# Performance work log

Hardware: AMD Instinct MI355X
Metric: run time of the kernel (lower is better)

The kernel has to match this reference:

```python
import jax, jax.numpy as jnp
import numpy as np

LORA_SCALING = 1.0 / 4.0  # lora_alpha / lora_rank
NUM_HEADS = 16
HEAD_DIM = 64
ROPE_BASE = 20000.0


def rotate_half(x):
    x1, x2 = jnp.split(x, 2, axis=-1)
    return jnp.concatenate([-x2, x1], axis=-1)


def setup_inputs() -> dict:
    key = jax.random.key(0)
    ks = jax.random.split(key, 8)
    B, S, D = 8, 1024, 1024
    hidden_states = jax.random.normal(ks[0], (B, S, D), jnp.float32)
    attention_mask = jnp.zeros((B, 1, 1, S), jnp.float32)
    # real rotary tables (HF style: duplicated half-dim freqs)
    inv_freq = 1.0 / (ROPE_BASE ** (jnp.arange(0, HEAD_DIM, 2, dtype=jnp.float32) / HEAD_DIM))
    t = jnp.arange(S, dtype=jnp.float32)
    freqs = jnp.outer(t, inv_freq)                      # [S, hd/2]
    emb = jnp.concatenate([freqs, freqs], axis=-1)      # [S, hd]
    cos = jnp.broadcast_to(jnp.cos(emb)[None], (B, S, HEAD_DIM))
    sin = jnp.broadcast_to(jnp.sin(emb)[None], (B, S, HEAD_DIM))
    adapter_mask = jax.random.randint(ks[1], (B,), 0, 5, jnp.int32)
    Wqkv_weight = jax.random.normal(ks[2], (3 * D, D), jnp.float32) * 0.02
    Wqkv_bias = jax.random.normal(ks[3], (3 * D,), jnp.float32) * 0.02
    lora_A = jax.random.normal(ks[4], (5, 4, D), jnp.float32) * 0.02
    lora_B = jax.random.normal(ks[5], (5, 3 * D, 4), jnp.float32) * 0.02
    return dict(hidden_states=hidden_states, attention_mask=attention_mask,
                cos=cos, sin=sin, adapter_mask=adapter_mask,
                Wqkv_weight=Wqkv_weight, Wqkv_bias=Wqkv_bias,
                lora_A=lora_A, lora_B=lora_B)


def reference(hidden_states, attention_mask, cos, sin, adapter_mask,
              Wqkv_weight, Wqkv_bias, lora_A, lora_B):
    B, S, D = hidden_states.shape
    H, hd = NUM_HEADS, HEAD_DIM
    # fused QKV projection with per-task LoRA (gather adapters per batch row)
    base = jnp.einsum('bsd,od->bso', hidden_states, Wqkv_weight) + Wqkv_bias
    A_t = lora_A[adapter_mask]                    # [B, r, D]
    B_t = lora_B[adapter_mask]                    # [B, 3D, r]
    lo = jnp.einsum('bsd,brd->bsr', hidden_states, A_t)
    delta = jnp.einsum('bsr,bor->bso', lo, B_t) * LORA_SCALING
    qkv = (base + delta).reshape(B, S, 3, H, hd)
    q = qkv[:, :, 0].transpose(0, 2, 1, 3)        # [B,H,S,hd]
    k = qkv[:, :, 1].transpose(0, 2, 1, 3)
    v = qkv[:, :, 2].transpose(0, 2, 1, 3)
    # inline RoPE
    c = cos[:, None, :, :]
    s = sin[:, None, :, :]
    q = q * c + rotate_half(q) * s
    k = k * c + rotate_half(k) * s
    # eager SDPA
    scaling = hd ** -0.5
    scores = jnp.einsum('bhqd,bhkd->bhqk', q, k) * scaling + attention_mask
    attn = jax.nn.softmax(scores, axis=-1)
    out = jnp.einsum('bhqk,bhkd->bhqd', attn, v)
    return out.transpose(0, 2, 1, 3).reshape(B, S, H * hd)
```

## Files before the change

### kernel.cpp

```cpp
#include <hip/hip_runtime.h>
#include <hip/hip_bf16.h>
#include <stdint.h>

typedef __attribute__((ext_vector_type(8))) short short8;
typedef __attribute__((ext_vector_type(4))) float f32x4;
typedef unsigned short ushort_t;

#define MFMA16(a, b, c) __builtin_amdgcn_mfma_f32_16x16x32_bf16((a), (b), (c), 0, 0, 0)
#define EXP2F(x) __builtin_amdgcn_exp2f(x)
#define BAR() __builtin_amdgcn_s_barrier()


__device__ __forceinline__ float bf2f(unsigned short u) {
    union { unsigned int i; float f; } x; x.i = ((unsigned int)u) << 16; return x.f;
}
__device__ __forceinline__ unsigned short f2bf(float f) {
    union { float f; unsigned int i; } x; x.f = f;
    unsigned int i = x.i;
    i = i + 0x7FFFu + ((i >> 16) & 1u);
    return (unsigned short)(i >> 16);
}
__device__ __forceinline__ unsigned int pack2(float a, float b) {
    return (unsigned int)f2bf(a) | ((unsigned int)f2bf(b) << 16);
}
__device__ __forceinline__ void glds16(const void* gsrc, void* ldst) {
    __builtin_amdgcn_global_load_lds(
        (const __attribute__((address_space(1))) unsigned int*)gsrc,
        (__attribute__((address_space(3))) unsigned int*)ldst, 16, 0, 0);
}

__global__ __launch_bounds__(64) void prep_kernel(
    const float* __restrict__ hidden,
    const float* __restrict__ W,
    const float* __restrict__ loraA,
    const int* __restrict__ adapter_mask,
    ushort_t* __restrict__ Hb,
    ushort_t* __restrict__ Wb,
    float4* __restrict__ lo)
{
    int blk = blockIdx.x;
    int lane = threadIdx.x;
    if (blk < 8192) {
        int b = blk >> 10;
        int a = adapter_mask[b];
        const float* hp = hidden + (size_t)blk * 1024 + lane * 16;
        float hv[16];
        for (int j = 0; j < 16; ++j) hv[j] = hp[j];
        uint4 p0, p1;
        p0.x = pack2(hv[0], hv[1]);  p0.y = pack2(hv[2], hv[3]);
        p0.z = pack2(hv[4], hv[5]);  p0.w = pack2(hv[6], hv[7]);
        p1.x = pack2(hv[8], hv[9]);  p1.y = pack2(hv[10], hv[11]);
        p1.z = pack2(hv[12], hv[13]); p1.w = pack2(hv[14], hv[15]);
        uint4* hd = (uint4*)(Hb + (size_t)blk * 1024 + lane * 16);
        hd[0] = p0; hd[1] = p1;
        const float* Ap = loraA + (size_t)a * 4096 + lane * 16;
        float acc[4];
        for (int r = 0; r < 4; ++r) {
            const float* ap = Ap + r * 1024;
            float s = 0.f;
            for (int j = 0; j < 16; ++j) s += hv[j] * ap[j];
            acc[r] = s;
        }
        for (int off = 32; off > 0; off >>= 1)
            for (int r = 0; r < 4; ++r) acc[r] += __shfl_xor(acc[r], off);
        if (lane == 0) lo[blk] = make_float4(acc[0], acc[1], acc[2], acc[3]);
    } else {
        int row = blk - 8192;
        const float* wp = W + (size_t)row * 1024 + lane * 16;
        float wv[16];
        for (int j = 0; j < 16; ++j) wv[j] = wp[j];
        uint4 p0, p1;
        p0.x = pack2(wv[0], wv[1]);  p0.y = pack2(wv[2], wv[3]);
        p0.z = pack2(wv[4], wv[5]);  p0.w = pack2(wv[6], wv[7]);
        p1.x = pack2(wv[8], wv[9]);  p1.y = pack2(wv[10], wv[11]);
        p1.z = pack2(wv[12], wv[13]); p1.w = pack2(wv[14], wv[15]);
        uint4* wd = (uint4*)(Wb + (size_t)row * 1024 + lane * 16);
        wd[0] = p0; wd[1] = p1;
    }
}

__global__ __launch_bounds__(512, 2) void qkv_gemm_kernel(
    const ushort_t* __restrict__ Hb,
    const ushort_t* __restrict__ Wb,
    const float* __restrict__ bias,
    const float4* __restrict__ lo,
    const float* __restrict__ loraB,
    const int* __restrict__ adapter_mask,
    const float* __restrict__ cosp,
    const float* __restrict__ sinp,
    ushort_t* __restrict__ qw,
    ushort_t* __restrict__ kw,
    ushort_t* __restrict__ vt)
{
    __shared__ __align__(16) ushort_t As[2][16384];
    __shared__ __align__(16) ushort_t Bs[2][16384];
    int tid = threadIdx.x;
    int wave = tid >> 6, lane = tid & 63, quad = lane >> 4, l16 = lane & 15;
    int wm = wave >> 2, wn = wave & 3;

    int wg = (blockIdx.x & 7) * 48 + (blockIdx.x >> 3);
    int bx = wg % 12, by = wg / 12;
    int n0 = bx * 256;
    int m0 = by * 256;

    int r_ = tid >> 3, c_ = (tid & 7) ^ (r_ & 7);
    const ushort_t* pA0 = Hb + (size_t)(m0 +   0 + r_) * 1024 + c_ * 8;
    const ushort_t* pA1 = Hb + (size_t)(m0 +  64 + r_) * 1024 + c_ * 8;
    const ushort_t* pA2 = Hb + (size_t)(m0 + 128 + r_) * 1024 + c_ * 8;
    const ushort_t* pA3 = Hb + (size_t)(m0 + 192 + r_) * 1024 + c_ * 8;
    const ushort_t* pB0 = Wb + (size_t)(n0 +   0 + r_) * 1024 + c_ * 8;
    const ushort_t* pB1 = Wb + (size_t)(n0 +  64 + r_) * 1024 + c_ * 8;
    const ushort_t* pB2 = Wb + (size_t)(n0 + 128 + r_) * 1024 + c_ * 8;
    const ushort_t* pB3 = Wb + (size_t)(n0 + 192 + r_) * 1024 + c_ * 8;
    char* stA0 = (char*)&As[0][0] + wave * 1024;
    char* stB0 = (char*)&Bs[0][0] + wave * 1024;

    f32x4 acc[8][4];
#pragma unroll
    for (int i = 0; i < 8; ++i)
#pragma unroll
        for (int j = 0; j < 4; ++j) acc[i][j] = (f32x4)0.f;

    glds16(pB0, stB0);          glds16(pB1, stB0 + 8192);
    glds16(pB2, stB0 + 16384);  glds16(pB3, stB0 + 24576);
    glds16(pA0, stA0);          glds16(pA1, stA0 + 8192);
    glds16(pA2, stA0 + 16384);  glds16(pA3, stA0 + 24576);
    glds16(pB0 + 64, stB0 + 32768);          glds16(pB1 + 64, stB0 + 32768 + 8192);
    glds16(pB2 + 64, stB0 + 32768 + 16384);  glds16(pB3 + 64, stB0 + 32768 + 24576);

#pragma unroll 2
    for (int t = 0; t < 16; ++t) {
        int cur = t & 1;
        const char* rdA = (const char*)&As[0][0] + cur * 32768;
        const char* rdB = (const char*)&Bs[0][0] + cur * 32768;
        char* sA = stA0 + (cur ^ 1) * 32768;
        char* sB = stB0 + cur * 32768;
        int kA = (t + 1) << 6;
        int kB = (t + 2) << 6;

        if (t < 15) { asm volatile("s_waitcnt vmcnt(4)" ::: "memory"); }
        else        { asm volatile("s_waitcnt vmcnt(0)" ::: "memory"); }
        BAR();
        if (t < 15) {
            glds16(pA0 + kA, sA);          glds16(pA1 + kA, sA + 8192);
            glds16(pA2 + kA, sA + 16384);  glds16(pA3 + kA, sA + 24576);
        }
        short8 bfr[4][2];
#pragma unroll
        for (int ni = 0; ni < 4; ++ni) {
            int rb = ni * 16 + l16;
            bfr[ni][0] = *(const short8*)(rdB + wn * 8192 + (rb * 8 + ((quad    ) ^ (rb & 7))) * 16);
            bfr[ni][1] = *(const short8*)(rdB + wn * 8192 + (rb * 8 + ((quad + 4) ^ (rb & 7))) * 16);
        }
        asm volatile("s_waitcnt lgkmcnt(0)" ::: "memory");
        BAR();
        if (t < 14) {
            glds16(pB0 + kB, sB);          glds16(pB1 + kB, sB + 8192);
            glds16(pB2 + kB, sB + 16384);  glds16(pB3 + kB, sB + 24576);
        }
        __builtin_amdgcn_s_setprio(1);
#pragma unroll
        for (int mi = 0; mi < 8; ++mi) {
            int u = wm * 2 + (mi >> 2);
            int rr = (mi & 3) * 16 + l16;
            short8 a0 = *(const short8*)(rdA + u * 8192 + (rr * 8 + ((quad    ) ^ (rr & 7))) * 16);
            short8 a1 = *(const short8*)(rdA + u * 8192 + (rr * 8 + ((quad + 4) ^ (rr & 7))) * 16);
            acc[mi][0] = MFMA16(a0, bfr[0][0], acc[mi][0]);
            acc[mi][1] = MFMA16(a0, bfr[1][0], acc[mi][1]);
            acc[mi][2] = MFMA16(a0, bfr[2][0], acc[mi][2]);
            acc[mi][3] = MFMA16(a0, bfr[3][0], acc[mi][3]);
            acc[mi][0] = MFMA16(a1, bfr[0][1], acc[mi][0]);
            acc[mi][1] = MFMA16(a1, bfr[1][1], acc[mi][1]);
            acc[mi][2] = MFMA16(a1, bfr[2][1], acc[mi][2]);
            acc[mi][3] = MFMA16(a1, bfr[3][1], acc[mi][3]);
        }
        __builtin_amdgcn_s_setprio(0);
    }

    int t_qkv = n0 >> 10;
    int b = m0 >> 10;
    int a_idx = adapter_mask[b];
    float bi[4], bb[4][4];
    int cpos[4], chh[4];
#pragma unroll
    for (int ni = 0; ni < 4; ++ni) {
        int c = n0 + wn * 64 + ni * 16 + l16;
        bi[ni] = bias[c];
        const float* Bp = loraB + ((size_t)a_idx * 3072 + c) * 4;
        bb[ni][0] = Bp[0]; bb[ni][1] = Bp[1]; bb[ni][2] = Bp[2]; bb[ni][3] = Bp[3];
        cpos[ni] = c & 63; chh[ni] = (c >> 6) & 15;
    }
#pragma unroll
    for (int mi = 0; mi < 8; ++mi) {
        float vals[4][4];
        int mrow0 = m0 + wm * 128 + mi * 16 + quad * 4;
#pragma unroll
        for (int r = 0; r < 4; ++r) {
            float4 lov = lo[mrow0 + r];
#pragma unroll
            for (int ni = 0; ni < 4; ++ni)
                vals[r][ni] = acc[mi][ni][r] + bi[ni]
                      + 0.25f * (lov.x * bb[ni][0] + lov.y * bb[ni][1]
                               + lov.z * bb[ni][2] + lov.w * bb[ni][3]);
        }
        int s0 = mrow0 & 1023;
        if (t_qkv < 2) {
#pragma unroll
            for (int r = 0; r < 4; ++r) {
                int s = s0 + r;
                size_t cb = ((size_t)b * 1024 + s) * 64;
                float cA = cosp[cb + l16],      sA_ = sinp[cb + l16];
                float cB = cosp[cb + 16 + l16], sB_ = sinp[cb + 16 + l16];
                float w0 = vals[r][0] * cA - vals[r][2] * sA_;
                float w2 = vals[r][2] * cA + vals[r][0] * sA_;
                float w1 = vals[r][1] * cB - vals[r][3] * sB_;
                float w3 = vals[r][3] * cB + vals[r][1] * sB_;
                float v[4] = {w0, w1, w2, w3};
#pragma unroll
                for (int ni = 0; ni < 4; ++ni) {
                    size_t bh = (size_t)b * 16 + chh[ni];
                    ushort_t ob = f2bf(v[ni]);
                    if (t_qkv == 0) qw[(bh * 1024 + s) * 64 + cpos[ni]] = ob;
                    else            kw[(bh * 1024 + s) * 64 + cpos[ni]] = ob;
                }
            }
        } else {
#pragma unroll
            for (int ni = 0; ni < 4; ++ni) {
                uint2 pk;
                pk.x = pack2(vals[0][ni], vals[1][ni]);
                pk.y = pack2(vals[2][ni], vals[3][ni]);
                size_t bh = (size_t)b * 16 + chh[ni];
                *(uint2*)&vt[(bh * 64 + cpos[ni]) * 1024 + s0] = pk;
            }
        }
    }
}

__global__ __launch_bounds__(256) void attn_kernel(
    const ushort_t* __restrict__ qw,
    const ushort_t* __restrict__ kw,
    const ushort_t* __restrict__ vt,
    const float* __restrict__ mask,
    float* __restrict__ out)
{
    __shared__ __align__(16) ushort_t Kt[3][4096];
    __shared__ __align__(16) ushort_t Vt[3][4096];
    __shared__ __align__(16) ushort_t Ps[4][32][72];
    __shared__ float mlds[1024];
    const float KSCALE = 0.125f * 1.44269504f;
    int tid = threadIdx.x;
    int wave = tid >> 6, lane = tid & 63, quad = lane >> 4, l16 = lane & 15;
    int id = blockIdx.x;
    int qt = id >> 7;
    int bh = id & 127;
    int b = bh >> 4, h = bh & 15;
    size_t base = (size_t)bh * 65536;
    int q0 = qt * 128 + wave * 32;

    for (int i = tid; i < 1024; i += 256) mlds[i] = mask[b * 1024 + i] * 1.44269504f;

    const ushort_t* kbase = kw + base;
    const ushort_t* vbase = vt + base;

    int n0 = tid, n1 = tid + 256;
    int r0 = n0 >> 3, c0 = (n0 & 7) ^ (r0 & 7);
    int r1 = n1 >> 3, c1 = (n1 & 7) ^ (r1 & 7);

    short8 qf[2][2];
    for (int mt = 0; mt < 2; ++mt)
        for (int kt = 0; kt < 2; ++kt)
            qf[mt][kt] = *(const short8*)(qw + base + (size_t)(q0 + mt * 16 + l16) * 64 + kt * 32 + quad * 8);

    f32x4 oacc[2][4], sum_acc[2];
    for (int mt = 0; mt < 2; ++mt) {
        sum_acc[mt] = (f32x4)0.f;
        for (int nt = 0; nt < 4; ++nt) oacc[mt][nt] = (f32x4)0.f;
    }

    short8 ones;
    for (int j = 0; j < 8; ++j) ones[j] = (short)0x3F80;

    __syncthreads();

    int koff[4][2], voff[4][2];
    for (int nt = 0; nt < 4; ++nt)
        for (int kt = 0; kt < 2; ++kt) {
            int rr = nt * 16 + l16;
            int cc = (kt * 4 + quad) ^ (rr & 7);
            koff[nt][kt] = (rr * 8 + cc) * 8;
            voff[nt][kt] = (rr * 8 + cc) * 8;
        }

    {
        char* kd = (char*)&Kt[0][0] + wave * 1024;
        char* vd = (char*)&Vt[0][0] + wave * 1024;
        glds16(kbase + (size_t)r0 * 64 + c0 * 8, kd);
        glds16(kbase + (size_t)r1 * 64 + c1 * 8, kd + 4096);
        glds16(vbase + (size_t)r0 * 1024 + c0 * 8, vd);
        glds16(vbase + (size_t)r1 * 1024 + c1 * 8, vd + 4096);
        kd = (char*)&Kt[1][0] + wave * 1024;
        vd = (char*)&Vt[1][0] + wave * 1024;
        glds16(kbase + (size_t)(64 + r0) * 64 + c0 * 8, kd);
        glds16(kbase + (size_t)(64 + r1) * 64 + c1 * 8, kd + 4096);
        glds16(vbase + (size_t)r0 * 1024 + 64 + c0 * 8, vd);
        glds16(vbase + (size_t)r1 * 1024 + 64 + c1 * 8, vd + 4096);
    }

    const ushort_t* kR  = &Kt[0][0];  const ushort_t* vR  = &Vt[0][0];
    const ushort_t* kN1 = &Kt[1][0];  const ushort_t* vN1 = &Vt[1][0];
    const ushort_t* kN2 = &Kt[2][0];  const ushort_t* vN2 = &Vt[2][0];

    for (int it = 0; it < 16; ++it) {
        int kt0 = it * 64;
        if (it < 15) { asm volatile("s_waitcnt vmcnt(4)" ::: "memory"); }
        else         { asm volatile("s_waitcnt vmcnt(0)" ::: "memory"); }
        BAR();
        __builtin_amdgcn_sched_barrier(0);
        if (it < 14) {
            int kn = kt0 + 128;
            char* kd = (char*)kN2 + wave * 1024;
            char* vd = (char*)vN2 + wave * 1024;
            glds16(kbase + (size_t)(kn + r0) * 64 + c0 * 8, kd);
            glds16(kbase + (size_t)(kn + r1) * 64 + c1 * 8, kd + 4096);
            glds16(vbase + (size_t)r0 * 1024 + kn + c0 * 8, vd);
            glds16(vbase + (size_t)r1 * 1024 + kn + c1 * 8, vd + 4096);
        }
        short8 kf[4][2];
        for (int nt = 0; nt < 4; ++nt)
            for (int kt = 0; kt < 2; ++kt)
                kf[nt][kt] = *(const short8*)&kR[koff[nt][kt]];
        f32x4 sacc[2][4];
        for (int mt = 0; mt < 2; ++mt)
            for (int nt = 0; nt < 4; ++nt) {
                f32x4 z = (f32x4)0.f;
                z = MFMA16(qf[mt][0], kf[nt][0], z);
                z = MFMA16(qf[mt][1], kf[nt][1], z);
                sacc[mt][nt] = z;
            }
        float mv[4];
        for (int nt = 0; nt < 4; ++nt) mv[nt] = mlds[kt0 + nt * 16 + l16];
        for (int mt = 0; mt < 2; ++mt)
            for (int nt = 0; nt < 4; ++nt)
                for (int r = 0; r < 4; ++r) {
                    float p = EXP2F(sacc[mt][nt][r] * KSCALE + mv[nt]);
                    Ps[wave][mt * 16 + quad * 4 + r][nt * 16 + l16] = f2bf(p);
                }
        short8 pf[2][2];
        for (int mt = 0; mt < 2; ++mt)
            for (int kt = 0; kt < 2; ++kt)
                pf[mt][kt] = *(const short8*)&Ps[wave][mt * 16 + l16][kt * 32 + quad * 8];
        short8 vf[4][2];
        for (int nt = 0; nt < 4; ++nt)
            for (int kt = 0; kt < 2; ++kt)
                vf[nt][kt] = *(const short8*)&vR[voff[nt][kt]];
        for (int mt = 0; mt < 2; ++mt) {
            for (int nt = 0; nt < 4; ++nt) {
                oacc[mt][nt] = MFMA16(pf[mt][0], vf[nt][0], oacc[mt][nt]);
                oacc[mt][nt] = MFMA16(pf[mt][1], vf[nt][1], oacc[mt][nt]);
            }
            sum_acc[mt] = MFMA16(pf[mt][0], ones, sum_acc[mt]);
            sum_acc[mt] = MFMA16(pf[mt][1], ones, sum_acc[mt]);
        }
        const ushort_t* tk = kR; kR = kN1; kN1 = kN2; kN2 = tk;
        const ushort_t* tv = vR; vR = vN1; vN1 = vN2; vN2 = tv;
    }

    for (int mt = 0; mt < 2; ++mt) {
        for (int r = 0; r < 4; ++r) {
            float inv = 1.f / sum_acc[mt][r];
            int s = q0 + mt * 16 + quad * 4 + r;
            size_t ob = ((size_t)b * 1024 + s) * 1024 + h * 64;
            for (int nt = 0; nt < 4; ++nt)
                out[ob + nt * 16 + l16] = oacc[mt][nt][r] * inv;
        }
    }
}

extern "C" void kernel_launch(void* const* d_in, const int* in_sizes, int n_in,
                              void* d_out, int out_size, void* d_ws, size_t ws_size,
                              hipStream_t stream)
{
    const float* hidden = (const float*)d_in[0];
    const float* mask   = (const float*)d_in[1];
    const float* cosp   = (const float*)d_in[2];
    const float* sinp   = (const float*)d_in[3];
    const int* adapter_mask = (const int*)d_in[4];
    const float* W      = (const float*)d_in[5];
    const float* bias   = (const float*)d_in[6];
    const float* loraA  = (const float*)d_in[7];
    const float* loraB  = (const float*)d_in[8];
    float* out = (float*)d_out;

    char* ws = (char*)d_ws;
    float4* lo = (float4*)ws;
    ushort_t* qw = (ushort_t*)(ws + (1 << 20));
    ushort_t* kw = qw + (size_t)8 * 16 * 1024 * 64;
    ushort_t* vt = kw + (size_t)8 * 16 * 1024 * 64;

    ushort_t* Hb = (ushort_t*)d_out;
    ushort_t* Wb = Hb + (size_t)8192 * 1024;

    prep_kernel<<<11264, 64, 0, stream>>>(hidden, W, loraA, adapter_mask, Hb, Wb, lo);
    qkv_gemm_kernel<<<384, 512, 0, stream>>>(Hb, Wb, bias, lo, loraB, adapter_mask,
                                             cosp, sinp, qw, kw, vt);
    attn_kernel<<<1024, 256, 0, stream>>>(qw, kw, vt, mask, out);
}
```

Measured before the change: 251.0 us.

## Shrink QKV GEMM tiles to 256x128 with BK=32 and 4-wave blocks

Reworks the QKV projection GEMM from 256x256 tiles with 8 waves and a K-step of 64 into 256x128 tiles with 4 waves and a K-step of 32, launching 768 blocks instead of 384. LDS use per block drops, the XOR swizzle changes to match the 64-byte rows, and up to three blocks may now share a CU. The aim is better occupancy and less tail imbalance. In exchange, each B tile is reused less, the loop runs twice as many iterations with barriers, and the MFMA priority hints are removed.

```diff
diff --git a/kernel.cpp b/kernel.cpp
--- a/kernel.cpp
+++ b/kernel.cpp
@@ -79,7 +79,7 @@
     }
 }
 
-__global__ __launch_bounds__(512, 2) void qkv_gemm_kernel(
+__global__ __launch_bounds__(256, 3) void qkv_gemm_kernel(
     const ushort_t* __restrict__ Hb,
     const ushort_t* __restrict__ Wb,
     const float* __restrict__ bias,
@@ -92,28 +92,31 @@
     ushort_t* __restrict__ kw,
     ushort_t* __restrict__ vt)
 {
-    __shared__ __align__(16) ushort_t As[2][16384];
-    __shared__ __align__(16) ushort_t Bs[2][16384];
+    __shared__ __align__(16) ushort_t As[2][8192];
+    __shared__ __align__(16) ushort_t Bs[2][4096];
     int tid = threadIdx.x;
     int wave = tid >> 6, lane = tid & 63, quad = lane >> 4, l16 = lane & 15;
-    int wm = wave >> 2, wn = wave & 3;
-
-    int wg = (blockIdx.x & 7) * 48 + (blockIdx.x >> 3);
-    int bx = wg % 12, by = wg / 12;
-    int n0 = bx * 256;
+    int wm = wave >> 1, wn = wave & 1;
+
+    int wg = (blockIdx.x & 7) * 96 + (blockIdx.x >> 3);
+    int bx = wg % 24, by = wg / 24;
+    int n0 = bx * 128;
     int m0 = by * 256;
 
-    int r_ = tid >> 3, c_ = (tid & 7) ^ (r_ & 7);
-    const ushort_t* pA0 = Hb + (size_t)(m0 +   0 + r_) * 1024 + c_ * 8;
-    const ushort_t* pA1 = Hb + (size_t)(m0 +  64 + r_) * 1024 + c_ * 8;
-    const ushort_t* pA2 = Hb + (size_t)(m0 + 128 + r_) * 1024 + c_ * 8;
-    const ushort_t* pA3 = Hb + (size_t)(m0 + 192 + r_) * 1024 + c_ * 8;
-    const ushort_t* pB0 = Wb + (size_t)(n0 +   0 + r_) * 1024 + c_ * 8;
-    const ushort_t* pB1 = Wb + (size_t)(n0 +  64 + r_) * 1024 + c_ * 8;
-    const ushort_t* pB2 = Wb + (size_t)(n0 + 128 + r_) * 1024 + c_ * 8;
-    const ushort_t* pB3 = Wb + (size_t)(n0 + 192 + r_) * 1024 + c_ * 8;
-    char* stA0 = (char*)&As[0][0] + wave * 1024;
-    char* stB0 = (char*)&Bs[0][0] + wave * 1024;
+    int rr = tid >> 2;
+    int cg = (tid & 3) ^ ((tid >> 3) & 3);
+    const ushort_t* pA0 = Hb + (size_t)(m0 +   0 + rr) * 1024 + cg * 8;
+    const ushort_t* pA1 = Hb + (size_t)(m0 +  64 + rr) * 1024 + cg * 8;
+    const ushort_t* pA2 = Hb + (size_t)(m0 + 128 + rr) * 1024 + cg * 8;
+    const ushort_t* pA3 = Hb + (size_t)(m0 + 192 + rr) * 1024 + cg * 8;
+    const ushort_t* pB0 = Wb + (size_t)(n0 +   0 + rr) * 1024 + cg * 8;
+    const ushort_t* pB1 = Wb + (size_t)(n0 +  64 + rr) * 1024 + cg * 8;
+    char* stA = (char*)&As[0][0] + wave * 1024;
+    char* stB = (char*)&Bs[0][0] + wave * 1024;
+
+    int slotoff = (quad ^ ((l16 >> 1) & 3)) * 16;
+    int bA = (wm * 128 + l16) * 64 + slotoff;
+    int bB = (wn * 64 + l16) * 64 + slotoff;
 
     f32x4 acc[8][4];
 #pragma unroll
@@ -121,60 +124,45 @@
 #pragma unroll
         for (int j = 0; j < 4; ++j) acc[i][j] = (f32x4)0.f;
 
-    glds16(pB0, stB0);          glds16(pB1, stB0 + 8192);
-    glds16(pB2, stB0 + 16384);  glds16(pB3, stB0 + 24576);
-    glds16(pA0, stA0);          glds16(pA1, stA0 + 8192);
-    glds16(pA2, stA0 + 16384);  glds16(pA3, stA0 + 24576);
-    glds16(pB0 + 64, stB0 + 32768);          glds16(pB1 + 64, stB0 + 32768 + 8192);
-    glds16(pB2 + 64, stB0 + 32768 + 16384);  glds16(pB3 + 64, stB0 + 32768 + 24576);
+    glds16(pB0, stB);          glds16(pB1, stB + 4096);
+    glds16(pA0, stA);          glds16(pA1, stA + 4096);
+    glds16(pA2, stA + 8192);   glds16(pA3, stA + 12288);
+    glds16(pB0 + 32, stB + 8192);  glds16(pB1 + 32, stB + 8192 + 4096);
 
 #pragma unroll 2
-    for (int t = 0; t < 16; ++t) {
+    for (int t = 0; t < 32; ++t) {
         int cur = t & 1;
-        const char* rdA = (const char*)&As[0][0] + cur * 32768;
-        const char* rdB = (const char*)&Bs[0][0] + cur * 32768;
-        char* sA = stA0 + (cur ^ 1) * 32768;
-        char* sB = stB0 + cur * 32768;
-        int kA = (t + 1) << 6;
-        int kB = (t + 2) << 6;
-
-        if (t < 15) { asm volatile("s_waitcnt vmcnt(4)" ::: "memory"); }
+        const char* rdA = (const char*)&As[0][0] + cur * 16384;
+        const char* rdB = (const char*)&Bs[0][0] + cur * 8192;
+        char* sA = stA + (cur ^ 1) * 16384;
+        char* sB = stB + cur * 8192;
+        int kA = (t + 1) * 32;
+        int kB = (t + 2) * 32;
+
+        if (t < 31) { asm volatile("s_waitcnt vmcnt(2)" ::: "memory"); }
         else        { asm volatile("s_waitcnt vmcnt(0)" ::: "memory"); }
         BAR();
-        if (t < 15) {
-            glds16(pA0 + kA, sA);          glds16(pA1 + kA, sA + 8192);
-            glds16(pA2 + kA, sA + 16384);  glds16(pA3 + kA, sA + 24576);
-        }
-        short8 bfr[4][2];
-#pragma unroll
-        for (int ni = 0; ni < 4; ++ni) {
-            int rb = ni * 16 + l16;
-            bfr[ni][0] = *(const short8*)(rdB + wn * 8192 + (rb * 8 + ((quad    ) ^ (rb & 7))) * 16);
-            bfr[ni][1] = *(const short8*)(rdB + wn * 8192 + (rb * 8 + ((quad + 4) ^ (rb & 7))) * 16);
-        }
+        if (t < 31) {
+            glds16(pA0 + kA, sA);          glds16(pA1 + kA, sA + 4096);
+            glds16(pA2 + kA, sA + 8192);   glds16(pA3 + kA, sA + 12288);
+        }
+        short8 bfr[4];
+#pragma unroll
+        for (int ni = 0; ni < 4; ++ni)
+            bfr[ni] = *(const short8*)(rdB + bB + ni * 1024);
         asm volatile("s_waitcnt lgkmcnt(0)" ::: "memory");
         BAR();
-        if (t < 14) {
-            glds16(pB0 + kB, sB);          glds16(pB1 + kB, sB + 8192);
-            glds16(pB2 + kB, sB + 16384);  glds16(pB3 + kB, sB + 24576);
-        }
-        __builtin_amdgcn_s_setprio(1);
+        if (t < 30) {
+            glds16(pB0 + kB, sB);          glds16(pB1 + kB, sB + 4096);
+        }
 #pragma unroll
         for (int mi = 0; mi < 8; ++mi) {
-            int u = wm * 2 + (mi >> 2);
-            int rr = (mi & 3) * 16 + l16;
-            short8 a0 = *(const short8*)(rdA + u * 8192 + (rr * 8 + ((quad    ) ^ (rr & 7))) * 16);
-            short8 a1 = *(const short8*)(rdA + u * 8192 + (rr * 8 + ((quad + 4) ^ (rr & 7))) * 16);
-            acc[mi][0] = MFMA16(a0, bfr[0][0], acc[mi][0]);
-            acc[mi][1] = MFMA16(a0, bfr[1][0], acc[mi][1]);
-            acc[mi][2] = MFMA16(a0, bfr[2][0], acc[mi][2]);
-            acc[mi][3] = MFMA16(a0, bfr[3][0], acc[mi][3]);
-            acc[mi][0] = MFMA16(a1, bfr[0][1], acc[mi][0]);
-            acc[mi][1] = MFMA16(a1, bfr[1][1], acc[mi][1]);
-            acc[mi][2] = MFMA16(a1, bfr[2][1], acc[mi][2]);
-            acc[mi][3] = MFMA16(a1, bfr[3][1], acc[mi][3]);
-        }
-        __builtin_amdgcn_s_setprio(0);
+            short8 a = *(const short8*)(rdA + bA + mi * 1024);
+            acc[mi][0] = MFMA16(a, bfr[0], acc[mi][0]);
+            acc[mi][1] = MFMA16(a, bfr[1], acc[mi][1]);
+            acc[mi][2] = MFMA16(a, bfr[2], acc[mi][2]);
+            acc[mi][3] = MFMA16(a, bfr[3], acc[mi][3]);
+        }
     }
 
     int t_qkv = n0 >> 10;
@@ -402,7 +390,7 @@
     ushort_t* Wb = Hb + (size_t)8192 * 1024;
 
     prep_kernel<<<11264, 64, 0, stream>>>(hidden, W, loraA, adapter_mask, Hb, Wb, lo);
-    qkv_gemm_kernel<<<384, 512, 0, stream>>>(Hb, Wb, bias, lo, loraB, adapter_mask,
+    qkv_gemm_kernel<<<768, 256, 0, stream>>>(Hb, Wb, bias, lo, loraB, adapter_mask,
                                              cosp, sinp, qw, kw, vt);
     attn_kernel<<<1024, 256, 0, stream>>>(qw, kw, vt, mask, out);
 }
```

Result: slower. 270.3 us (+7.7%).

## Load K/V fragments directly from global in attention and pack prep blocks

Applied to the files above, without the earlier changes.

The attention kernel drops its triple-buffered LDS staging of K and V tiles, including the async global-to-LDS loads, waitcnt and barriers. Each wave now reads its MFMA K and V fragments straight from global memory, relying on L1/L2 to serve the reuse across the four waves in a block. This removes barrier synchronisation and LDS traffic, but loses explicit prefetch overlap and may add redundant global reads. Separately, the prep kernel packs four 64-thread rows into one 256-thread block to cut the block count.

```diff
diff --git a/kernel.cpp b/kernel.cpp
--- a/kernel.cpp
+++ b/kernel.cpp
@@ -29,7 +29,7 @@
         (__attribute__((address_space(3))) unsigned int*)ldst, 16, 0, 0);
 }
 
-__global__ __launch_bounds__(64) void prep_kernel(
+__global__ __launch_bounds__(256) void prep_kernel(
     const float* __restrict__ hidden,
     const float* __restrict__ W,
     const float* __restrict__ loraA,
@@ -38,8 +38,9 @@
     ushort_t* __restrict__ Wb,
     float4* __restrict__ lo)
 {
-    int blk = blockIdx.x;
-    int lane = threadIdx.x;
+    int tid = threadIdx.x;
+    int blk = blockIdx.x * 4 + (tid >> 6);
+    int lane = tid & 63;
     if (blk < 8192) {
         int b = blk >> 10;
         int a = adapter_mask[b];
@@ -244,8 +245,6 @@
     const float* __restrict__ mask,
     float* __restrict__ out)
 {
-    __shared__ __align__(16) ushort_t Kt[3][4096];
-    __shared__ __align__(16) ushort_t Vt[3][4096];
     __shared__ __align__(16) ushort_t Ps[4][32][72];
     __shared__ float mlds[1024];
     const float KSCALE = 0.125f * 1.44269504f;
@@ -263,10 +262,6 @@
     const ushort_t* kbase = kw + base;
     const ushort_t* vbase = vt + base;
 
-    int n0 = tid, n1 = tid + 256;
-    int r0 = n0 >> 3, c0 = (n0 & 7) ^ (r0 & 7);
-    int r1 = n1 >> 3, c1 = (n1 & 7) ^ (r1 & 7);
-
     short8 qf[2][2];
     for (int mt = 0; mt < 2; ++mt)
         for (int kt = 0; kt < 2; ++kt)
@@ -283,53 +278,13 @@
 
     __syncthreads();
 
-    int koff[4][2], voff[4][2];
-    for (int nt = 0; nt < 4; ++nt)
-        for (int kt = 0; kt < 2; ++kt) {
-            int rr = nt * 16 + l16;
-            int cc = (kt * 4 + quad) ^ (rr & 7);
-            koff[nt][kt] = (rr * 8 + cc) * 8;
-            voff[nt][kt] = (rr * 8 + cc) * 8;
-        }
-
-    {
-        char* kd = (char*)&Kt[0][0] + wave * 1024;
-        char* vd = (char*)&Vt[0][0] + wave * 1024;
-        glds16(kbase + (size_t)r0 * 64 + c0 * 8, kd);
-        glds16(kbase + (size_t)r1 * 64 + c1 * 8, kd + 4096);
-        glds16(vbase + (size_t)r0 * 1024 + c0 * 8, vd);
-        glds16(vbase + (size_t)r1 * 1024 + c1 * 8, vd + 4096);
-        kd = (char*)&Kt[1][0] + wave * 1024;
-        vd = (char*)&Vt[1][0] + wave * 1024;
-        glds16(kbase + (size_t)(64 + r0) * 64 + c0 * 8, kd);
-        glds16(kbase + (size_t)(64 + r1) * 64 + c1 * 8, kd + 4096);
-        glds16(vbase + (size_t)r0 * 1024 + 64 + c0 * 8, vd);
-        glds16(vbase + (size_t)r1 * 1024 + 64 + c1 * 8, vd + 4096);
-    }
-
-    const ushort_t* kR  = &Kt[0][0];  const ushort_t* vR  = &Vt[0][0];
-    const ushort_t* kN1 = &Kt[1][0];  const ushort_t* vN1 = &Vt[1][0];
-    const ushort_t* kN2 = &Kt[2][0];  const ushort_t* vN2 = &Vt[2][0];
-
     for (int it = 0; it < 16; ++it) {
         int kt0 = it * 64;
-        if (it < 15) { asm volatile("s_waitcnt vmcnt(4)" ::: "memory"); }
-        else         { asm volatile("s_waitcnt vmcnt(0)" ::: "memory"); }
-        BAR();
-        __builtin_amdgcn_sched_barrier(0);
-        if (it < 14) {
-            int kn = kt0 + 128;
-            char* kd = (char*)kN2 + wave * 1024;
-            char* vd = (char*)vN2 + wave * 1024;
-            glds16(kbase + (size_t)(kn + r0) * 64 + c0 * 8, kd);
-            glds16(kbase + (size_t)(kn + r1) * 64 + c1 * 8, kd + 4096);
-            glds16(vbase + (size_t)r0 * 1024 + kn + c0 * 8, vd);
-            glds16(vbase + (size_t)r1 * 1024 + kn + c1 * 8, vd + 4096);
-        }
         short8 kf[4][2];
         for (int nt = 0; nt < 4; ++nt)
             for (int kt = 0; kt < 2; ++kt)
-                kf[nt][kt] = *(const short8*)&kR[koff[nt][kt]];
+                kf[nt][kt] = *(const short8*)(kbase
+                    + (size_t)(kt0 + nt * 16 + l16) * 64 + kt * 32 + quad * 8);
         f32x4 sacc[2][4];
         for (int mt = 0; mt < 2; ++mt)
             for (int nt = 0; nt < 4; ++nt) {
@@ -353,7 +308,8 @@
         short8 vf[4][2];
         for (int nt = 0; nt < 4; ++nt)
             for (int kt = 0; kt < 2; ++kt)
-                vf[nt][kt] = *(const short8*)&vR[voff[nt][kt]];
+                vf[nt][kt] = *(const short8*)(vbase
+                    + (size_t)(nt * 16 + l16) * 1024 + kt0 + kt * 32 + quad * 8);
         for (int mt = 0; mt < 2; ++mt) {
             for (int nt = 0; nt < 4; ++nt) {
                 oacc[mt][nt] = MFMA16(pf[mt][0], vf[nt][0], oacc[mt][nt]);
@@ -362,8 +318,6 @@
             sum_acc[mt] = MFMA16(pf[mt][0], ones, sum_acc[mt]);
             sum_acc[mt] = MFMA16(pf[mt][1], ones, sum_acc[mt]);
         }
-        const ushort_t* tk = kR; kR = kN1; kN1 = kN2; kN2 = tk;
-        const ushort_t* tv = vR; vR = vN1; vN1 = vN2; vN2 = tv;
     }
 
     for (int mt = 0; mt < 2; ++mt) {
@@ -401,7 +355,7 @@
     ushort_t* Hb = (ushort_t*)d_out;
     ushort_t* Wb = Hb + (size_t)8192 * 1024;
 
-    prep_kernel<<<11264, 64, 0, stream>>>(hidden, W, loraA, adapter_mask, Hb, Wb, lo);
+    prep_kernel<<<2816, 256, 0, stream>>>(hidden, W, loraA, adapter_mask, Hb, Wb, lo);
     qkv_gemm_kernel<<<384, 512, 0, stream>>>(Hb, Wb, bias, lo, loraB, adapter_mask,
                                              cosp, sinp, qw, kw, vt);
     attn_kernel<<<1024, 256, 0, stream>>>(qw, kw, vt, mask, out);
```

Measured after the change: 336.0 us. 33.8% more time.
